# Performance work log

Measured on AMD Instinct MI355X. Metric: run time of the kernel, lower is better.

The kernel has to match this reference:

```python
import jax, jax.numpy as jnp
import numpy as np

D_MODEL = 1024
NUM_HEADS = 16
D_K = D_MODEL // NUM_HEADS


def setup_inputs() -> dict:
    key = jax.random.key(0)
    ks = jax.random.split(key, 11)
    B, S = 2, 2048
    scale = 1.0 / np.sqrt(D_MODEL)
    inp = {
        "query": jax.random.normal(ks[0], (B, S, D_MODEL), jnp.float32),
        "key": jax.random.normal(ks[1], (B, S, D_MODEL), jnp.float32),
        "value": jax.random.normal(ks[2], (B, S, D_MODEL), jnp.float32),
        "Wq": jax.random.normal(ks[3], (D_MODEL, D_MODEL), jnp.float32) * scale,
        "bq": jnp.zeros((D_MODEL,), jnp.float32),
        "Wk": jax.random.normal(ks[4], (D_MODEL, D_MODEL), jnp.float32) * scale,
        "bk": jnp.zeros((D_MODEL,), jnp.float32),
        "Wv": jax.random.normal(ks[5], (D_MODEL, D_MODEL), jnp.float32) * scale,
        "bv": jnp.zeros((D_MODEL,), jnp.float32),
        "Wo": jax.random.normal(ks[6], (D_MODEL, D_MODEL), jnp.float32) * scale,
        "bo": jnp.zeros((D_MODEL,), jnp.float32),
    }
    return inp


def _split_heads(x):
    B, S, _ = x.shape
    return x.reshape(B, S, NUM_HEADS, D_K).transpose(0, 2, 1, 3)  # [B,H,S,d_k]


def reference(query, key, value, Wq, bq, Wk, bk, Wv, bv, Wo, bo):
    # Linear projections (torch Linear: x @ W.T + b)
    q = _split_heads(query @ Wq.T + bq)
    k = _split_heads(key @ Wk.T + bk)
    v = _split_heads(value @ Wv.T + bv)
    scores = jnp.einsum("bhqd,bhkd->bhqk", q, k) / jnp.sqrt(jnp.float32(D_K))
    probs = jax.nn.softmax(scores, axis=-1)
    out = jnp.einsum("bhqk,bhkd->bhqd", probs, v)  # [B,H,S,d_k]
    B, H, S, _ = out.shape
    out = out.transpose(0, 2, 1, 3).reshape(B, S, D_MODEL)
    return out @ Wo.T + bo
```

## Files before the change

### kernel.cpp

```cpp
#include <hip/hip_runtime.h>

#define D_MODEL 1024
#define NHEADS  16
#define DK      64
#define SEQ     2048
#define NBATCH  2
#define MTOT    (NBATCH * SEQ)

typedef _Float16 f16;
typedef _Float16 f16x4 __attribute__((ext_vector_type(4)));
typedef _Float16 f16x8 __attribute__((ext_vector_type(8)));
typedef float    f32x4 __attribute__((ext_vector_type(4)));
typedef float    f32x16 __attribute__((ext_vector_type(16)));

#define LOG2E 1.44269504088896340736f

__global__ __launch_bounds__(256) void cvt_f32_to_f16(
    const float* __restrict__ q, const float* __restrict__ k, const float* __restrict__ v,
    const float* __restrict__ wq, const float* __restrict__ wk,
    const float* __restrict__ wv, const float* __restrict__ wo,
    f16* __restrict__ qf, f16* __restrict__ kf, f16* __restrict__ vf,
    f16* __restrict__ wqh, f16* __restrict__ wkh, f16* __restrict__ wvh, f16* __restrict__ woh)
{
    const int z = blockIdx.y;
    const float* src; f16* dst; int n4;
    if (z == 0)      { src = q;  dst = qf;  n4 = MTOT * D_MODEL / 4; }
    else if (z == 1) { src = k;  dst = kf;  n4 = MTOT * D_MODEL / 4; }
    else if (z == 2) { src = v;  dst = vf;  n4 = MTOT * D_MODEL / 4; }
    else if (z == 3) { src = wq; dst = wqh; n4 = D_MODEL * D_MODEL / 4; }
    else if (z == 4) { src = wk; dst = wkh; n4 = D_MODEL * D_MODEL / 4; }
    else if (z == 5) { src = wv; dst = wvh; n4 = D_MODEL * D_MODEL / 4; }
    else             { src = wo; dst = woh; n4 = D_MODEL * D_MODEL / 4; }
    for (int i = blockIdx.x * 256 + threadIdx.x; i < n4; i += gridDim.x * 256) {
        float4 t = ((const float4*)src)[i];
        f16x4 o = {(f16)t.x, (f16)t.y, (f16)t.z, (f16)t.w};
        ((f16x4*)dst)[i] = o;
    }
}

__device__ __forceinline__ void gemm128_core(
    const f16* __restrict__ A, const f16* __restrict__ Wm,
    int m0, int n0, int kbeg, int kend, f32x16 (&acc)[2][2])
{
    __shared__ __align__(16) f16 As[4096];
    __shared__ __align__(16) f16 Bs[4096];

    const int t    = threadIdx.x;
    const int lane = t & 63;
    const int w    = t >> 6;
    const int l31  = lane & 31, kg = lane >> 5;
    const int wr   = w >> 1,    wc = w & 1;

    size_t offA[2], offB[2];
#pragma unroll
    for (int jj = 0; jj < 2; ++jj) {
        int s  = (w * 2 + jj) * 64 + lane;
        int ko = s >> 7, m = s & 127;
        offA[jj] = (size_t)(m0 + m) * D_MODEL + ko * 8;
        offB[jj] = (size_t)(n0 + m) * D_MODEL + ko * 8;
    }
    const int jb = __builtin_amdgcn_readfirstlane(w * 1024);

#pragma unroll
    for (int i = 0; i < 2; ++i)
#pragma unroll
        for (int j = 0; j < 2; ++j)
#pragma unroll
            for (int r = 0; r < 16; ++r) acc[i][j][r] = 0.f;

    auto* ldsA = (__attribute__((address_space(3))) f16*)As;
    auto* ldsB = (__attribute__((address_space(3))) f16*)Bs;

    for (int k0 = kbeg; k0 < kend; k0 += 32) {
#pragma unroll
        for (int jj = 0; jj < 2; ++jj) {
            __builtin_amdgcn_global_load_lds(
                (const __attribute__((address_space(1))) void*)(A + offA[jj] + k0),
                (__attribute__((address_space(3))) void*)(ldsA + jb + jj * 512),
                16, 0, 0);
            __builtin_amdgcn_global_load_lds(
                (const __attribute__((address_space(1))) void*)(Wm + offB[jj] + k0),
                (__attribute__((address_space(3))) void*)(ldsB + jb + jj * 512),
                16, 0, 0);
        }
        __syncthreads();

#pragma unroll
        for (int step = 0; step < 2; ++step) {
            const int kk = kg + 2 * step;
            f16x8 aF[2], bF[2];
#pragma unroll
            for (int ti = 0; ti < 2; ++ti) {
                aF[ti] = *(const f16x8*)&As[(kk * 128 + wr * 64 + ti * 32 + l31) * 8];
                bF[ti] = *(const f16x8*)&Bs[(kk * 128 + wc * 64 + ti * 32 + l31) * 8];
            }
#pragma unroll
            for (int ti = 0; ti < 2; ++ti)
#pragma unroll
                for (int tj = 0; tj < 2; ++tj)
                    acc[ti][tj] = __builtin_amdgcn_mfma_f32_32x32x16_f16(
                        aF[ti], bF[tj], acc[ti][tj], 0, 0, 0);
        }
        __syncthreads();
    }
}

__global__ __launch_bounds__(256, 3) void qkv_gemm(
    const f16* __restrict__ Qf, const f16* __restrict__ Kf, const f16* __restrict__ Vf,
    const f16* __restrict__ Wqh, const f16* __restrict__ Wkh, const f16* __restrict__ Wvh,
    const float* __restrict__ bq, const float* __restrict__ bk, const float* __restrict__ bv,
    f16* __restrict__ Qh, f16* __restrict__ Kh, f16* __restrict__ Vt)
{
    const int z = blockIdx.z;
    const f16*   A    = z == 0 ? Qf  : z == 1 ? Kf  : Vf;
    const f16*   Wm   = z == 0 ? Wqh : z == 1 ? Wkh : Wvh;
    const float* bias = z == 0 ? bq  : z == 1 ? bk  : bv;

    const int m0 = blockIdx.x * 128, n0 = blockIdx.y * 128;
    f32x16 acc[2][2];
    gemm128_core(A, Wm, m0, n0, 0, D_MODEL, acc);

    const int t = threadIdx.x, lane = t & 63, w = t >> 6;
    const int l31 = lane & 31, kg = lane >> 5;
    const int wr = w >> 1, wc = w & 1;

    if (z < 2) {
        f16* Out = z == 0 ? Qh : Kh;
        const float sc = z == 0 ? 0.125f * LOG2E : 1.0f;
#pragma unroll
        for (int tj = 0; tj < 2; ++tj) {
            const int col = n0 + wc * 64 + tj * 32 + l31;
            const float bc = bias[col];
#pragma unroll
            for (int ti = 0; ti < 2; ++ti)
#pragma unroll
                for (int r = 0; r < 16; ++r) {
                    const int row = m0 + wr * 64 + ti * 32 + (r & 3) + 8 * (r >> 2) + 4 * kg;
                    Out[(size_t)row * D_MODEL + col] = (f16)((acc[ti][tj][r] + bc) * sc);
                }
        }
    } else {
#pragma unroll
        for (int tj = 0; tj < 2; ++tj) {
            const int col = n0 + wc * 64 + tj * 32 + l31;
            const float bc = bias[col];
            const int h = col >> 6, d = col & 63;
#pragma unroll
            for (int ti = 0; ti < 2; ++ti)
#pragma unroll
                for (int r = 0; r < 16; ++r) {
                    const int row = m0 + wr * 64 + ti * 32 + (r & 3) + 8 * (r >> 2) + 4 * kg;
                    const int bb = row >> 11, s = row & (SEQ - 1);
                    Vt[(size_t)((bb * NHEADS + h) * DK + d) * SEQ + s] = (f16)(acc[ti][tj][r] + bc);
                }
        }
    }
}

__global__ __launch_bounds__(256, 3) void oproj_splitk(
    const f16* __restrict__ A, const f16* __restrict__ Wm,
    float* __restrict__ P0, float* __restrict__ P1)
{
    const int z = blockIdx.z;
    const int m0 = blockIdx.x * 128, n0 = blockIdx.y * 128;
    f32x16 acc[2][2];
    gemm128_core(A, Wm, m0, n0, z * 512, z * 512 + 512, acc);

    float* Out = z == 0 ? P0 : P1;
    const int t = threadIdx.x, lane = t & 63, w = t >> 6;
    const int l31 = lane & 31, kg = lane >> 5;
    const int wr = w >> 1, wc = w & 1;
#pragma unroll
    for (int tj = 0; tj < 2; ++tj) {
        const int col = n0 + wc * 64 + tj * 32 + l31;
#pragma unroll
        for (int ti = 0; ti < 2; ++ti)
#pragma unroll
            for (int r = 0; r < 16; ++r) {
                const int row = m0 + wr * 64 + ti * 32 + (r & 3) + 8 * (r >> 2) + 4 * kg;
                Out[(size_t)row * D_MODEL + col] = acc[ti][tj][r];
            }
    }
}

__global__ __launch_bounds__(256) void reduce_bias(
    const float* __restrict__ P0, const float* __restrict__ P1,
    const float* __restrict__ bias, float* __restrict__ Out)
{
    const int n4 = MTOT * D_MODEL / 4;
    for (int i = blockIdx.x * 256 + threadIdx.x; i < n4; i += gridDim.x * 256) {
        float4 a = ((const float4*)P0)[i];
        float4 b = ((const float4*)P1)[i];
        float4 c = ((const float4*)bias)[i & 255];
        float4 o = {a.x + b.x + c.x, a.y + b.y + c.y,
                    a.z + b.z + c.z, a.w + b.w + c.w};
        ((float4*)Out)[i] = o;
    }
}

__global__ __launch_bounds__(256, 4) void mha_mfma_v8(
    const f16* __restrict__ Qh, const f16* __restrict__ Kh,
    const f16* __restrict__ Vt, f16* __restrict__ Op, float* __restrict__ sp)
{
    __shared__ __align__(16) f16 Ks[4096];
    __shared__ __align__(16) f16 Vc[4096];
    __shared__ __align__(16) f16 Ps[64 * 68];

    const int t    = threadIdx.x;
    const int w    = t >> 6;
    const int lane = t & 63;
    const int quad = lane >> 4, l15 = lane & 15;

    const int bh = blockIdx.x, qt = blockIdx.y, third = blockIdx.z;
    const int b  = bh >> 4,    h  = bh & 15;
    const int q0 = qt * 128;

    f16x8 aQ[2][2];
#pragma unroll
    for (int s = 0; s < 2; ++s)
#pragma unroll
        for (int c = 0; c < 2; ++c)
            aQ[s][c] = *(const f16x8*)&Qh[
                (size_t)(b * SEQ + q0 + w * 32 + s * 16 + l15) * D_MODEL
                + h * DK + c * 32 + quad * 8];

    const f16* gK[2]; const f16* gV[2]; int ldst[2];
#pragma unroll
    for (int jj = 0; jj < 2; ++jj) {
        const int kc = w * 2 + jj;
        gK[jj] = Kh + (size_t)(b * SEQ + lane) * D_MODEL + h * DK + kc * 8;
        gV[jj] = Vt + (size_t)(bh * DK + lane) * SEQ + kc * 8;
        ldst[jj] = __builtin_amdgcn_readfirstlane(kc * 512);
    }
    auto* ldsK = (__attribute__((address_space(3))) f16*)Ks;
    auto* ldsV = (__attribute__((address_space(3))) f16*)Vc;

    const f16x8 onesB = {(f16)1.f, (f16)1.f, (f16)1.f, (f16)1.f,
                         (f16)1.f, (f16)1.f, (f16)1.f, (f16)1.f};

    f32x4 o[2][4];
#pragma unroll
    for (int s = 0; s < 2; ++s)
#pragma unroll
        for (int j = 0; j < 4; ++j) o[s][j] = (f32x4){0.f, 0.f, 0.f, 0.f};
    f32x4 sacc[2] = {(f32x4){0.f, 0.f, 0.f, 0.f}, (f32x4){0.f, 0.f, 0.f, 0.f}};

    const int kt0   = third * 11;
    const int ktend = (third == 2) ? 32 : kt0 + 11;
    for (int kt = kt0; kt < ktend; ++kt) {
#pragma unroll
        for (int jj = 0; jj < 2; ++jj) {
            __builtin_amdgcn_global_load_lds(
                (const __attribute__((address_space(1))) void*)(gK[jj] + (size_t)kt * 64 * D_MODEL),
                (__attribute__((address_space(3))) void*)(ldsK + ldst[jj]), 16, 0, 0);
            __builtin_amdgcn_global_load_lds(
                (const __attribute__((address_space(1))) void*)(gV[jj] + kt * 64),
                (__attribute__((address_space(3))) void*)(ldsV + ldst[jj]), 16, 0, 0);
        }
        __syncthreads();

        f16x8 bK[4][2], bV[4][2];
#pragma unroll
        for (int f = 0; f < 4; ++f)
#pragma unroll
            for (int c = 0; c < 2; ++c) {
                const int slot = ((c * 4 + quad) * 64 + f * 16 + l15) * 8;
                bK[f][c] = *(const f16x8*)&Ks[slot];
                bV[f][c] = *(const f16x8*)&Vc[slot];
            }

#pragma unroll
        for (int s = 0; s < 2; ++s) {
            f32x4 sc[4];
#pragma unroll
            for (int f = 0; f < 4; ++f) {
                f32x4 a = (f32x4){0.f, 0.f, 0.f, 0.f};
                a = __builtin_amdgcn_mfma_f32_16x16x32_f16(aQ[s][0], bK[f][0], a, 0, 0, 0);
                a = __builtin_amdgcn_mfma_f32_16x16x32_f16(aQ[s][1], bK[f][1], a, 0, 0, 0);
                sc[f] = a;
            }

#pragma unroll
            for (int f = 0; f < 4; ++f)
#pragma unroll
                for (int r = 0; r < 4; ++r)
                    sc[f][r] = __builtin_exp2f(sc[f][r]);

#pragma unroll
            for (int f = 0; f < 4; ++f)
#pragma unroll
                for (int r = 0; r < 4; ++r)
                    Ps[(w * 16 + quad * 4 + r) * 68 + f * 16 + l15] = (f16)sc[f][r];

            f16x8 aP[2];
#pragma unroll
            for (int c = 0; c < 2; ++c) {
                const int off = (w * 16 + l15) * 68 + c * 32 + quad * 8;
                f16x4 lo = *(const f16x4*)&Ps[off];
                f16x4 hi = *(const f16x4*)&Ps[off + 4];
                aP[c] = __builtin_shufflevector(lo, hi, 0, 1, 2, 3, 4, 5, 6, 7);
            }

#pragma unroll
            for (int j = 0; j < 4; ++j) {
                o[s][j] = __builtin_amdgcn_mfma_f32_16x16x32_f16(aP[0], bV[j][0], o[s][j], 0, 0, 0);
                o[s][j] = __builtin_amdgcn_mfma_f32_16x16x32_f16(aP[1], bV[j][1], o[s][j], 0, 0, 0);
            }
            sacc[s] = __builtin_amdgcn_mfma_f32_16x16x32_f16(aP[0], onesB, sacc[s], 0, 0, 0);
            sacc[s] = __builtin_amdgcn_mfma_f32_16x16x32_f16(aP[1], onesB, sacc[s], 0, 0, 0);
        }
        __syncthreads();
    }

#pragma unroll
    for (int s = 0; s < 2; ++s)
#pragma unroll
        for (int r = 0; r < 4; ++r) {
            const int qrow = q0 + w * 32 + s * 16 + quad * 4 + r;
            const size_t base = ((size_t)(third * 32 + bh) * SEQ + qrow) * DK;
#pragma unroll
            for (int j = 0; j < 4; ++j)
                Op[base + j * 16 + l15] = (f16)o[s][j][r];
            if (l15 == 0)
                sp[(size_t)(third * 32 + bh) * SEQ + qrow] = sacc[s][r];
        }
}

__global__ __launch_bounds__(256) void mha_combine(
    const f16* __restrict__ Op, const float* __restrict__ sp,
    f16* __restrict__ ATh)
{
    const int gid = blockIdx.x * 256 + threadIdx.x;
    const int d4 = gid & 15;
    const int q  = (gid >> 4) & (SEQ - 1);
    const int bh = gid >> 15;
    const int b = bh >> 4, h = bh & 15;

    float acc[4] = {0.f, 0.f, 0.f, 0.f};
    float ssum = 0.f;
#pragma unroll
    for (int tpart = 0; tpart < 3; ++tpart) {
        const size_t idx = ((size_t)(tpart * 32 + bh) * SEQ + q) * DK + d4 * 4;
        f16x4 a = *(const f16x4*)&Op[idx];
#pragma unroll
        for (int m = 0; m < 4; ++m) acc[m] += (float)a[m];
        ssum += sp[(size_t)(tpart * 32 + bh) * SEQ + q];
    }
    const float inv = 1.f / ssum;
    f16x4 r;
#pragma unroll
    for (int m = 0; m < 4; ++m) r[m] = (f16)(acc[m] * inv);
    *(f16x4*)&ATh[((size_t)(b * SEQ + q)) * D_MODEL + h * DK + d4 * 4] = r;
}

extern "C" void kernel_launch(void* const* d_in, const int* in_sizes, int n_in,
                              void* d_out, int out_size, void* d_ws, size_t ws_size,
                              hipStream_t stream)
{
    const float* query = (const float*)d_in[0];
    const float* key   = (const float*)d_in[1];
    const float* value = (const float*)d_in[2];
    const float* Wq    = (const float*)d_in[3];
    const float* bq    = (const float*)d_in[4];
    const float* Wk    = (const float*)d_in[5];
    const float* bk    = (const float*)d_in[6];
    const float* Wv    = (const float*)d_in[7];
    const float* bv    = (const float*)d_in[8];
    const float* Wo    = (const float*)d_in[9];
    const float* bo    = (const float*)d_in[10];
    float* out = (float*)d_out;

    f16* Qf  = (f16*)d_ws;
    f16* Kf  = Qf  + (size_t)MTOT * D_MODEL;
    f16* Vf  = Kf  + (size_t)MTOT * D_MODEL;
    f16* Wqh = Vf  + (size_t)MTOT * D_MODEL;
    f16* Wkh = Wqh + (size_t)D_MODEL * D_MODEL;
    f16* Wvh = Wkh + (size_t)D_MODEL * D_MODEL;
    f16* Woh = Wvh + (size_t)D_MODEL * D_MODEL;
    f16* Qh  = Woh + (size_t)D_MODEL * D_MODEL;
    f16* Kh  = Qh  + (size_t)MTOT * D_MODEL;
    f16* Vt  = Kh  + (size_t)MTOT * D_MODEL;
    f16* ATh = Vt  + (size_t)MTOT * D_MODEL;

    f16*   Op = Qf;
    float* sp = (float*)Wqh;
    float* P0 = (float*)Qf;
    float* P1 = (float*)Qh;

    cvt_f32_to_f16<<<dim3(1024, 7), 256, 0, stream>>>(
        query, key, value, Wq, Wk, Wv, Wo, Qf, Kf, Vf, Wqh, Wkh, Wvh, Woh);

    qkv_gemm<<<dim3(MTOT / 128, D_MODEL / 128, 3), 256, 0, stream>>>(
        Qf, Kf, Vf, Wqh, Wkh, Wvh, bq, bk, bv, Qh, Kh, Vt);

    mha_mfma_v8<<<dim3(NBATCH * NHEADS, SEQ / 128, 3), 256, 0, stream>>>(
        Qh, Kh, Vt, Op, sp);

    mha_combine<<<dim3(MTOT * D_MODEL / 4 / 256), 256, 0, stream>>>(Op, sp, ATh);

    oproj_splitk<<<dim3(MTOT / 128, D_MODEL / 128, 2), 256, 0, stream>>>(ATh, Woh, P0, P1);

    reduce_bias<<<dim3(1024), 256, 0, stream>>>(P0, P1, bo, out);
}
```

Measured before the change: 263.8 us.

## Fuse fp32->fp16 activation conversion into QKV GEMM and drop split-K output projection

The QKV GEMM now loads fp32 activations straight into LDS and converts them to fp16 while building MFMA fragments, so the separate conversion pass over the activations and its fp16 copies go away. Only the weights are still pre-converted. The output projection switches from a split-K GEMM plus reduce/bias kernel to a single direct GEMM with 128x64 tiles that adds the bias in its epilogue, removing the partial-sum round trip. The trade-offs are twice the LDS traffic for A in the QKV GEMM plus in-loop conversion work, and a longer K loop per block in the output projection.

```diff
diff --git a/kernel.cpp b/kernel.cpp
--- a/kernel.cpp
+++ b/kernel.cpp
@@ -15,22 +15,16 @@
 
 #define LOG2E 1.44269504088896340736f
 
-__global__ __launch_bounds__(256) void cvt_f32_to_f16(
-    const float* __restrict__ q, const float* __restrict__ k, const float* __restrict__ v,
+__global__ __launch_bounds__(256) void cvt_w_f16(
     const float* __restrict__ wq, const float* __restrict__ wk,
     const float* __restrict__ wv, const float* __restrict__ wo,
-    f16* __restrict__ qf, f16* __restrict__ kf, f16* __restrict__ vf,
-    f16* __restrict__ wqh, f16* __restrict__ wkh, f16* __restrict__ wvh, f16* __restrict__ woh)
+    f16* __restrict__ wqh, f16* __restrict__ wkh,
+    f16* __restrict__ wvh, f16* __restrict__ woh)
 {
     const int z = blockIdx.y;
-    const float* src; f16* dst; int n4;
-    if (z == 0)      { src = q;  dst = qf;  n4 = MTOT * D_MODEL / 4; }
-    else if (z == 1) { src = k;  dst = kf;  n4 = MTOT * D_MODEL / 4; }
-    else if (z == 2) { src = v;  dst = vf;  n4 = MTOT * D_MODEL / 4; }
-    else if (z == 3) { src = wq; dst = wqh; n4 = D_MODEL * D_MODEL / 4; }
-    else if (z == 4) { src = wk; dst = wkh; n4 = D_MODEL * D_MODEL / 4; }
-    else if (z == 5) { src = wv; dst = wvh; n4 = D_MODEL * D_MODEL / 4; }
-    else             { src = wo; dst = woh; n4 = D_MODEL * D_MODEL / 4; }
+    const float* src = z == 0 ? wq : z == 1 ? wk : z == 2 ? wv : wo;
+    f16* dst        = z == 0 ? wqh : z == 1 ? wkh : z == 2 ? wvh : woh;
+    const int n4 = D_MODEL * D_MODEL / 4;
     for (int i = blockIdx.x * 256 + threadIdx.x; i < n4; i += gridDim.x * 256) {
         float4 t = ((const float4*)src)[i];
         f16x4 o = {(f16)t.x, (f16)t.y, (f16)t.z, (f16)t.w};
@@ -38,12 +32,21 @@
     }
 }
 
-__device__ __forceinline__ void gemm128_core(
-    const f16* __restrict__ A, const f16* __restrict__ Wm,
-    int m0, int n0, int kbeg, int kend, f32x16 (&acc)[2][2])
-{
-    __shared__ __align__(16) f16 As[4096];
-    __shared__ __align__(16) f16 Bs[4096];
+__global__ __launch_bounds__(256, 3) void qkv_gemm(
+    const float* __restrict__ Q32, const float* __restrict__ K32, const float* __restrict__ V32,
+    const f16* __restrict__ Wqh, const f16* __restrict__ Wkh, const f16* __restrict__ Wvh,
+    const float* __restrict__ bq, const float* __restrict__ bk, const float* __restrict__ bv,
+    f16* __restrict__ Qh, f16* __restrict__ Kh, f16* __restrict__ Vt)
+{
+    __shared__ __align__(16) float As32[4096];
+    __shared__ __align__(16) f16   Bs[4096];
+
+    const int z = blockIdx.z;
+    const float* A32  = z == 0 ? Q32 : z == 1 ? K32 : V32;
+    const f16*   Wm   = z == 0 ? Wqh : z == 1 ? Wkh : Wvh;
+    const float* bias = z == 0 ? bq  : z == 1 ? bk  : bv;
+
+    const int m0 = blockIdx.x * 128, n0 = blockIdx.y * 128;
 
     const int t    = threadIdx.x;
     const int lane = t & 63;
@@ -51,16 +54,28 @@
     const int l31  = lane & 31, kg = lane >> 5;
     const int wr   = w >> 1,    wc = w & 1;
 
-    size_t offA[2], offB[2];
+    size_t offA[4];
+#pragma unroll
+    for (int jj = 0; jj < 4; ++jj) {
+        int s   = (w * 4 + jj) * 64 + lane;
+        int ko4 = s >> 7, m = s & 127;
+        offA[jj] = (size_t)(m0 + m) * D_MODEL + ko4 * 4;
+    }
+    const int jbA = __builtin_amdgcn_readfirstlane(w * 1024);
+
+    size_t offB[2];
 #pragma unroll
     for (int jj = 0; jj < 2; ++jj) {
         int s  = (w * 2 + jj) * 64 + lane;
         int ko = s >> 7, m = s & 127;
-        offA[jj] = (size_t)(m0 + m) * D_MODEL + ko * 8;
         offB[jj] = (size_t)(n0 + m) * D_MODEL + ko * 8;
     }
-    const int jb = __builtin_amdgcn_readfirstlane(w * 1024);
-
+    const int jbB = __builtin_amdgcn_readfirstlane(w * 1024);
+
+    auto* ldsA = (__attribute__((address_space(3))) float*)As32;
+    auto* ldsB = (__attribute__((address_space(3))) f16*)Bs;
+
+    f32x16 acc[2][2];
 #pragma unroll
     for (int i = 0; i < 2; ++i)
 #pragma unroll
@@ -68,21 +83,19 @@
 #pragma unroll
             for (int r = 0; r < 16; ++r) acc[i][j][r] = 0.f;
 
-    auto* ldsA = (__attribute__((address_space(3))) f16*)As;
-    auto* ldsB = (__attribute__((address_space(3))) f16*)Bs;
-
-    for (int k0 = kbeg; k0 < kend; k0 += 32) {
-#pragma unroll
-        for (int jj = 0; jj < 2; ++jj) {
+    for (int k0 = 0; k0 < D_MODEL; k0 += 32) {
+#pragma unroll
+        for (int jj = 0; jj < 4; ++jj)
             __builtin_amdgcn_global_load_lds(
-                (const __attribute__((address_space(1))) void*)(A + offA[jj] + k0),
-                (__attribute__((address_space(3))) void*)(ldsA + jb + jj * 512),
+                (const __attribute__((address_space(1))) void*)(A32 + offA[jj] + k0),
+                (__attribute__((address_space(3))) void*)(ldsA + jbA + jj * 256),
                 16, 0, 0);
+#pragma unroll
+        for (int jj = 0; jj < 2; ++jj)
             __builtin_amdgcn_global_load_lds(
                 (const __attribute__((address_space(1))) void*)(Wm + offB[jj] + k0),
-                (__attribute__((address_space(3))) void*)(ldsB + jb + jj * 512),
+                (__attribute__((address_space(3))) void*)(ldsB + jbB + jj * 512),
                 16, 0, 0);
-        }
         __syncthreads();
 
 #pragma unroll
@@ -91,7 +104,11 @@
             f16x8 aF[2], bF[2];
 #pragma unroll
             for (int ti = 0; ti < 2; ++ti) {
-                aF[ti] = *(const f16x8*)&As[(kk * 128 + wr * 64 + ti * 32 + l31) * 8];
+                const int m = wr * 64 + ti * 32 + l31;
+                float4 a0 = *(const float4*)&As32[((kk * 2 + 0) * 128 + m) * 4];
+                float4 a1 = *(const float4*)&As32[((kk * 2 + 1) * 128 + m) * 4];
+                aF[ti] = (f16x8){(f16)a0.x, (f16)a0.y, (f16)a0.z, (f16)a0.w,
+                                 (f16)a1.x, (f16)a1.y, (f16)a1.z, (f16)a1.w};
                 bF[ti] = *(const f16x8*)&Bs[(kk * 128 + wc * 64 + ti * 32 + l31) * 8];
             }
 #pragma unroll
@@ -103,26 +120,6 @@
         }
         __syncthreads();
     }
-}
-
-__global__ __launch_bounds__(256, 3) void qkv_gemm(
-    const f16* __restrict__ Qf, const f16* __restrict__ Kf, const f16* __restrict__ Vf,
-    const f16* __restrict__ Wqh, const f16* __restrict__ Wkh, const f16* __restrict__ Wvh,
-    const float* __restrict__ bq, const float* __restrict__ bk, const float* __restrict__ bv,
-    f16* __restrict__ Qh, f16* __restrict__ Kh, f16* __restrict__ Vt)
-{
-    const int z = blockIdx.z;
-    const f16*   A    = z == 0 ? Qf  : z == 1 ? Kf  : Vf;
-    const f16*   Wm   = z == 0 ? Wqh : z == 1 ? Wkh : Wvh;
-    const float* bias = z == 0 ? bq  : z == 1 ? bk  : bv;
-
-    const int m0 = blockIdx.x * 128, n0 = blockIdx.y * 128;
-    f32x16 acc[2][2];
-    gemm128_core(A, Wm, m0, n0, 0, D_MODEL, acc);
-
-    const int t = threadIdx.x, lane = t & 63, w = t >> 6;
-    const int l31 = lane & 31, kg = lane >> 5;
-    const int wr = w >> 1, wc = w & 1;
 
     if (z < 2) {
         f16* Out = z == 0 ? Qh : Kh;
@@ -157,45 +154,78 @@
     }
 }
 
-__global__ __launch_bounds__(256, 3) void oproj_splitk(
+__global__ __launch_bounds__(256, 2) void oproj_direct(
     const f16* __restrict__ A, const f16* __restrict__ Wm,
-    float* __restrict__ P0, float* __restrict__ P1)
-{
-    const int z = blockIdx.z;
-    const int m0 = blockIdx.x * 128, n0 = blockIdx.y * 128;
-    f32x16 acc[2][2];
-    gemm128_core(A, Wm, m0, n0, z * 512, z * 512 + 512, acc);
-
-    float* Out = z == 0 ? P0 : P1;
-    const int t = threadIdx.x, lane = t & 63, w = t >> 6;
-    const int l31 = lane & 31, kg = lane >> 5;
-    const int wr = w >> 1, wc = w & 1;
-#pragma unroll
-    for (int tj = 0; tj < 2; ++tj) {
-        const int col = n0 + wc * 64 + tj * 32 + l31;
-#pragma unroll
-        for (int ti = 0; ti < 2; ++ti)
-#pragma unroll
-            for (int r = 0; r < 16; ++r) {
-                const int row = m0 + wr * 64 + ti * 32 + (r & 3) + 8 * (r >> 2) + 4 * kg;
-                Out[(size_t)row * D_MODEL + col] = acc[ti][tj][r];
-            }
-    }
-}
-
-__global__ __launch_bounds__(256) void reduce_bias(
-    const float* __restrict__ P0, const float* __restrict__ P1,
     const float* __restrict__ bias, float* __restrict__ Out)
 {
-    const int n4 = MTOT * D_MODEL / 4;
-    for (int i = blockIdx.x * 256 + threadIdx.x; i < n4; i += gridDim.x * 256) {
-        float4 a = ((const float4*)P0)[i];
-        float4 b = ((const float4*)P1)[i];
-        float4 c = ((const float4*)bias)[i & 255];
-        float4 o = {a.x + b.x + c.x, a.y + b.y + c.y,
-                    a.z + b.z + c.z, a.w + b.w + c.w};
-        ((float4*)Out)[i] = o;
-    }
+    __shared__ __align__(16) f16 As[4096];
+    __shared__ __align__(16) f16 Bs[2048];
+
+    const int m0 = blockIdx.x * 128, n0 = blockIdx.y * 64;
+
+    const int t    = threadIdx.x;
+    const int lane = t & 63;
+    const int w    = t >> 6;
+    const int l31  = lane & 31, kg = lane >> 5;
+    const int wr   = w >> 1,    wc = w & 1;
+
+    size_t offA[2];
+#pragma unroll
+    for (int jj = 0; jj < 2; ++jj) {
+        int s  = (w * 2 + jj) * 64 + lane;
+        int ko = s >> 7, m = s & 127;
+        offA[jj] = (size_t)(m0 + m) * D_MODEL + ko * 8;
+    }
+    int sB = w * 64 + lane;
+    const size_t offB = (size_t)(n0 + (sB & 63)) * D_MODEL + (sB >> 6) * 8;
+
+    const int jbA = __builtin_amdgcn_readfirstlane(w * 1024);
+    const int jbB = __builtin_amdgcn_readfirstlane(w * 512);
+
+    auto* ldsA = (__attribute__((address_space(3))) f16*)As;
+    auto* ldsB = (__attribute__((address_space(3))) f16*)Bs;
+
+    f32x16 acc[2];
+#pragma unroll
+    for (int i = 0; i < 2; ++i)
+#pragma unroll
+        for (int r = 0; r < 16; ++r) acc[i][r] = 0.f;
+
+    for (int k0 = 0; k0 < D_MODEL; k0 += 32) {
+#pragma unroll
+        for (int jj = 0; jj < 2; ++jj)
+            __builtin_amdgcn_global_load_lds(
+                (const __attribute__((address_space(1))) void*)(A + offA[jj] + k0),
+                (__attribute__((address_space(3))) void*)(ldsA + jbA + jj * 512),
+                16, 0, 0);
+        __builtin_amdgcn_global_load_lds(
+            (const __attribute__((address_space(1))) void*)(Wm + offB + k0),
+            (__attribute__((address_space(3))) void*)(ldsB + jbB),
+            16, 0, 0);
+        __syncthreads();
+
+#pragma unroll
+        for (int step = 0; step < 2; ++step) {
+            const int kk = kg + 2 * step;
+            f16x8 bF = *(const f16x8*)&Bs[(kk * 64 + wc * 32 + l31) * 8];
+#pragma unroll
+            for (int ti = 0; ti < 2; ++ti) {
+                f16x8 aF = *(const f16x8*)&As[(kk * 128 + wr * 64 + ti * 32 + l31) * 8];
+                acc[ti] = __builtin_amdgcn_mfma_f32_32x32x16_f16(aF, bF, acc[ti], 0, 0, 0);
+            }
+        }
+        __syncthreads();
+    }
+
+    const int col = n0 + wc * 32 + l31;
+    const float bc = bias[col];
+#pragma unroll
+    for (int ti = 0; ti < 2; ++ti)
+#pragma unroll
+        for (int r = 0; r < 16; ++r) {
+            const int row = m0 + wr * 64 + ti * 32 + (r & 3) + 8 * (r >> 2) + 4 * kg;
+            Out[(size_t)row * D_MODEL + col] = acc[ti][r] + bc;
+        }
 }
 
 __global__ __launch_bounds__(256, 4) void mha_mfma_v8(
@@ -370,10 +400,9 @@
     const float* bo    = (const float*)d_in[10];
     float* out = (float*)d_out;
 
-    f16* Qf  = (f16*)d_ws;
-    f16* Kf  = Qf  + (size_t)MTOT * D_MODEL;
-    f16* Vf  = Kf  + (size_t)MTOT * D_MODEL;
-    f16* Wqh = Vf  + (size_t)MTOT * D_MODEL;
+    f16* Op  = (f16*)d_ws;
+    float* sp = (float*)(Op + (size_t)13 * 1024 * 1024);
+    f16* Wqh = (f16*)(sp + (size_t)256 * 1024);
     f16* Wkh = Wqh + (size_t)D_MODEL * D_MODEL;
     f16* Wvh = Wkh + (size_t)D_MODEL * D_MODEL;
     f16* Woh = Wvh + (size_t)D_MODEL * D_MODEL;
@@ -381,24 +410,31 @@
     f16* Kh  = Qh  + (size_t)MTOT * D_MODEL;
     f16* Vt  = Kh  + (size_t)MTOT * D_MODEL;
     f16* ATh = Vt  + (size_t)MTOT * D_MODEL;
-
-    f16*   Op = Qf;
-    float* sp = (float*)Wqh;
-    float* P0 = (float*)Qf;
-    float* P1 = (float*)Qh;
-
-    cvt_f32_to_f16<<<dim3(1024, 7), 256, 0, stream>>>(
-        query, key, value, Wq, Wk, Wv, Wo, Qf, Kf, Vf, Wqh, Wkh, Wvh, Woh);
+    {
+        f16* base = (f16*)d_ws;
+        Op  = base;
+        sp  = (float*)(base + (size_t)12582912);
+        Wqh = (f16*)((float*)sp + (size_t)196608);
+        Wkh = Wqh + (size_t)D_MODEL * D_MODEL;
+        Wvh = Wkh + (size_t)D_MODEL * D_MODEL;
+        Woh = Wvh + (size_t)D_MODEL * D_MODEL;
+        Qh  = Woh + (size_t)D_MODEL * D_MODEL;
+        Kh  = Qh  + (size_t)MTOT * D_MODEL;
+        Vt  = Kh  + (size_t)MTOT * D_MODEL;
+        ATh = Vt  + (size_t)MTOT * D_MODEL;
+    }
+
+    cvt_w_f16<<<dim3(128, 4), 256, 0, stream>>>(
+        Wq, Wk, Wv, Wo, Wqh, Wkh, Wvh, Woh);
 
     qkv_gemm<<<dim3(MTOT / 128, D_MODEL / 128, 3), 256, 0, stream>>>(
-        Qf, Kf, Vf, Wqh, Wkh, Wvh, bq, bk, bv, Qh, Kh, Vt);
+        query, key, value, Wqh, Wkh, Wvh, bq, bk, bv, Qh, Kh, Vt);
 
     mha_mfma_v8<<<dim3(NBATCH * NHEADS, SEQ / 128, 3), 256, 0, stream>>>(
         Qh, Kh, Vt, Op, sp);
 
     mha_combine<<<dim3(MTOT * D_MODEL / 4 / 256), 256, 0, stream>>>(Op, sp, ATh);
 
-    oproj_splitk<<<dim3(MTOT / 128, D_MODEL / 128, 2), 256, 0, stream>>>(ATh, Woh, P0, P1);
-
-    reduce_bias<<<dim3(1024), 256, 0, stream>>>(P0, P1, bo, out);
-}
+    oproj_direct<<<dim3(MTOT / 128, D_MODEL / 64), 256, 0, stream>>>(
+        ATh, Woh, bo, out);
+}
```

New measurement: 290.0 us. +9.9%, slower.
